# Performance work log

Hardware: AMD Instinct MI355X
Metric: run time of the kernel (lower is better)

Reference implementation:

```python
import jax, jax.numpy as jnp
import numpy as np

T, H, I, E = 8192, 1024, 2816, 8


def setup_inputs() -> dict:
    key = jax.random.key(0)
    k1, k2, k3, k4, k5 = jax.random.split(key, 5)
    s_in = 1.0 / np.sqrt(H)
    s_mid = 1.0 / np.sqrt(I)
    return {
        "x": jax.random.normal(k1, (T, H), dtype=jnp.float32),
        "expert_indices": jax.random.randint(k2, (T,), 0, E),
        "Wg": jax.random.normal(k3, (E, I, H), dtype=jnp.float32) * s_in,
        "Wu": jax.random.normal(k4, (E, I, H), dtype=jnp.float32) * s_in,
        "Wd": jax.random.normal(k5, (E, H, I), dtype=jnp.float32) * s_mid,
    }


def reference(x, expert_indices, Wg, Wu, Wd):
    # Faithful to TPMoEExperts.forward: per-expert 0/1 mask, dense SwiGLU MLP
    # over the full (masked) token batch, masked accumulate into output.
    output = jnp.zeros_like(x)
    for e in range(E):  # small fixed loop over experts (structurally distinct weights)
        mask = (expert_indices == e).astype(x.dtype)[:, None]  # [T,1]
        xi = x * mask                                           # [T,H]
        gate = jax.nn.silu(xi @ Wg[e].T)                        # [T,I]
        up = xi @ Wu[e].T                                       # [T,I]
        out_e = (gate * up) @ Wd[e].T                           # [T,H]
        output = output + out_e * mask
    return output
```

## Files before the change

### kernel.cpp

```cpp
#include <hip/hip_runtime.h>
#include <hip/hip_bf16.h>

#define T_TOK 8192
#define H_DIM 1024
#define I_DIM 2816
#define E_EXP 8

#define BK 64
#define MAXT (T_TOK / 256 + E_EXP)
#define GU_COLS (I_DIM / 128)
#define DN_COLS (H_DIM / 128)

typedef __bf16 bf16x8 __attribute__((ext_vector_type(8)));
typedef float f32x4 __attribute__((ext_vector_type(4)));

#define SWZ(r, bc) (((r) * (BK * 2)) + (((bc) ^ (((r) & 7) << 4))))

__device__ __forceinline__ void gload16(const void* g, void* l) {
  __builtin_amdgcn_global_load_lds((const __attribute__((address_space(1))) void*)g,
                                   (__attribute__((address_space(3))) void*)l, 16, 0, 0);
}

__device__ __forceinline__ bf16x8 cvt8(const float4& p0, const float4& p1) {
  bf16x8 v;
  v[0] = (__bf16)p0.x; v[1] = (__bf16)p0.y; v[2] = (__bf16)p0.z; v[3] = (__bf16)p0.w;
  v[4] = (__bf16)p1.x; v[5] = (__bf16)p1.y; v[6] = (__bf16)p1.z; v[7] = (__bf16)p1.w;
  return v;
}

__device__ __forceinline__ int xcd_swizzle(int id, int nwg) {
  const int q = nwg >> 3, r = nwg & 7;
  const int xcd = id & 7, j = id >> 3;
  return (xcd < r ? xcd * (q + 1) : r * (q + 1) + (xcd - r) * q) + j;
}

__global__ void k_count(const int* __restrict__ idx, int* __restrict__ counts) {
  int t = blockIdx.x * blockDim.x + threadIdx.x;
  if (t < T_TOK) atomicAdd(&counts[idx[t]], 1);
}

__global__ void k_tilesB(const int* __restrict__ counts, int* __restrict__ offsets,
                         int* __restrict__ tE, int* __restrict__ tB,
                         int* __restrict__ tEnd, int* __restrict__ nT) {
  if (threadIdx.x != 0 || blockIdx.x != 0) return;
  int off = 0, nt = 0;
  for (int e = 0; e < E_EXP; ++e) {
    offsets[e] = off;
    int c = counts[e];
    for (int b = 0; b < c; b += 256) { tE[nt] = e; tB[nt] = off + b; tEnd[nt] = off + c; ++nt; }
    off += c;
  }
  offsets[E_EXP] = off;
  *nT = nt;
}

__global__ void k_scatter(const int* __restrict__ idx, const int* __restrict__ offsets,
                          int* __restrict__ cursor, int* __restrict__ order) {
  int t = blockIdx.x * blockDim.x + threadIdx.x;
  if (t < T_TOK) {
    int e = idx[t];
    int p = offsets[e] + atomicAdd(&cursor[e], 1);
    order[p] = t;
  }
}

__global__ __launch_bounds__(256) void k_cvt3(const float* __restrict__ s0, const float* __restrict__ s1,
                                              const float* __restrict__ s2, __bf16* __restrict__ d0,
                                              __bf16* __restrict__ d1, __bf16* __restrict__ d2, int n8each) {
  int i = blockIdx.x * blockDim.x + threadIdx.x;
  int seg = i / n8each;
  int j = i - seg * n8each;
  if (seg >= 3) return;
  const float* s = seg == 0 ? s0 : (seg == 1 ? s1 : s2);
  __bf16* d = seg == 0 ? d0 : (seg == 1 ? d1 : d2);
  const float4 p0 = ((const float4*)s)[j * 2];
  const float4 p1 = ((const float4*)s)[j * 2 + 1];
  ((bf16x8*)d)[j] = cvt8(p0, p1);
}

__global__ __launch_bounds__(128) void k_xperm(const float* __restrict__ x,
                                               const int* __restrict__ order,
                                               __bf16* __restrict__ xp) {
  const int row = blockIdx.x;
  const int tok = order[row];
  const float* s = x + (size_t)tok * H_DIM + threadIdx.x * 8;
  const float4 p0 = ((const float4*)s)[0];
  const float4 p1 = ((const float4*)s)[1];
  *(bf16x8*)(xp + (size_t)row * H_DIM + threadIdx.x * 8) = cvt8(p0, p1);
}

__global__ __launch_bounds__(512, 2) void k_gateup7(
    const __bf16* __restrict__ xp, const __bf16* __restrict__ wg, const __bf16* __restrict__ wu,
    const int* __restrict__ tE, const int* __restrict__ tB,
    const int* __restrict__ tEnd, const int* __restrict__ nT, __bf16* __restrict__ hp) {
  const int nwg = *nT * GU_COLS;
  const int id = blockIdx.x;
  if (id >= nwg) return;
  const int wgid = xcd_swizzle(id, nwg);
  const int tile = wgid / GU_COLS;
  const int col = wgid - tile * GU_COLS;
  const int e = tE[tile];
  const int rowbase = tB[tile];
  const int rowEnd = tEnd[tile];
  const int nbase = col * 128;

  extern __shared__ __align__(16) unsigned char smem[];
  unsigned char* smA = smem;
  unsigned char* smG = smem + 65536;
  unsigned char* smU = smem + 98304;

  const int tid = threadIdx.x;
  const int lane = tid & 63;
  const int w = tid >> 6;
  const int wm = w & 3, wn = w >> 2;

  const int lr = lane >> 3;
  const int lc = (lane & 7) ^ lr;
  const __bf16* aS[4]; const __bf16* gS[2]; const __bf16* uS[2];
  int adst[4], gdst[2];
#pragma unroll
  for (int r = 0; r < 4; ++r) {
    const int rt = r * 64 + w * 8 + lr;
    aS[r] = xp + (size_t)(rowbase + rt) * H_DIM + lc * 8;
    adst[r] = rt * 128;
  }
#pragma unroll
  for (int r = 0; r < 2; ++r) {
    const int rt = r * 64 + w * 8 + lr;
    gS[r] = wg + ((size_t)e * I_DIM + nbase + rt) * H_DIM + lc * 8;
    uS[r] = wu + ((size_t)e * I_DIM + nbase + rt) * H_DIM + lc * 8;
    gdst[r] = rt * 128;
  }

  f32x4 accg[4][4], accu[4][4];
#pragma unroll
  for (int m = 0; m < 4; ++m)
#pragma unroll
    for (int n = 0; n < 4; ++n)
#pragma unroll
      for (int j = 0; j < 4; ++j) { accg[m][n][j] = 0.f; accu[m][n][j] = 0.f; }

  const int nK = H_DIM / BK;
#pragma unroll
  for (int r = 0; r < 4; ++r) gload16(aS[r], smA + adst[r]);
#pragma unroll
  for (int r = 0; r < 2; ++r) {
    gload16(gS[r], smG + gdst[r]);
    gload16(uS[r], smU + gdst[r]);
  }
  __syncthreads();

  int cur = 0;
  for (int kt = 0; kt < nK; ++kt) {
    if (kt + 1 < nK) {
      const int kof = (kt + 1) * BK;
      const int bA = (cur ^ 1) * 32768, bG = (cur ^ 1) * 16384;
#pragma unroll
      for (int r = 0; r < 4; ++r) gload16(aS[r] + kof, smA + bA + adst[r]);
#pragma unroll
      for (int r = 0; r < 2; ++r) {
        gload16(gS[r] + kof, smG + bG + gdst[r]);
        gload16(uS[r] + kof, smU + bG + gdst[r]);
      }
    }
    const unsigned char* A = smA + cur * 32768;
    const unsigned char* G = smG + cur * 16384;
    const unsigned char* U = smU + cur * 16384;
#pragma unroll
    for (int ks = 0; ks < 2; ++ks) {
      const int kc = ks * 64 + ((lane >> 4) * 16);
      bf16x8 a[4], bg[4], bu[4];
#pragma unroll
      for (int m = 0; m < 4; ++m)
        a[m] = *(const bf16x8*)(A + SWZ(wm * 64 + m * 16 + (lane & 15), kc));
#pragma unroll
      for (int n = 0; n < 4; ++n) {
        const int off = SWZ(wn * 64 + n * 16 + (lane & 15), kc);
        bg[n] = *(const bf16x8*)(G + off);
        bu[n] = *(const bf16x8*)(U + off);
      }
#pragma unroll
      for (int m = 0; m < 4; ++m)
#pragma unroll
        for (int n = 0; n < 4; ++n) {
          accg[m][n] = __builtin_amdgcn_mfma_f32_16x16x32_bf16(a[m], bg[n], accg[m][n], 0, 0, 0);
          accu[m][n] = __builtin_amdgcn_mfma_f32_16x16x32_bf16(a[m], bu[n], accu[m][n], 0, 0, 0);
        }
    }
    __syncthreads();
    cur ^= 1;
  }

#pragma unroll
  for (int m = 0; m < 4; ++m) {
    const int row0 = wm * 64 + m * 16 + (lane >> 4) * 4;
#pragma unroll
    for (int j = 0; j < 4; ++j) {
      const int gr = rowbase + row0 + j;
      if (gr < rowEnd) {
        __bf16* dst = hp + (size_t)gr * I_DIM + nbase;
#pragma unroll
        for (int n = 0; n < 4; ++n) {
          const int c2 = wn * 64 + n * 16 + (lane & 15);
          const float g = accg[m][n][j];
          const float u = accu[m][n][j];
          dst[c2] = (__bf16)(g / (1.f + __expf(-g)) * u);
        }
      }
    }
  }
}

__global__ __launch_bounds__(512, 2) void k_down7(
    const __bf16* __restrict__ hp, const __bf16* __restrict__ wd,
    const int* __restrict__ order, const int* __restrict__ tE, const int* __restrict__ tB,
    const int* __restrict__ tEnd, const int* __restrict__ nT, float* __restrict__ out) {
  const int nwg = *nT * DN_COLS;
  const int id = blockIdx.x;
  if (id >= nwg) return;
  const int wgid = xcd_swizzle(id, nwg);
  const int tile = wgid >> 3;
  const int col = wgid & 7;
  const int e = tE[tile];
  const int rowbase = tB[tile];
  const int rowEnd = tEnd[tile];
  const int nbase = col * 128;

  extern __shared__ __align__(16) unsigned char smem2[];
  unsigned char* smA = smem2;
  unsigned char* smB = smem2 + 65536;

  const int tid = threadIdx.x;
  const int lane = tid & 63;
  const int w = tid >> 6;
  const int wm = w & 3, wn = w >> 2;

  const int lr = lane >> 3;
  const int lc = (lane & 7) ^ lr;
  const __bf16* aS[4]; const __bf16* bS[2];
  int adst[4], bdst[2];
#pragma unroll
  for (int r = 0; r < 4; ++r) {
    const int rt = r * 64 + w * 8 + lr;
    aS[r] = hp + (size_t)(rowbase + rt) * I_DIM + lc * 8;
    adst[r] = rt * 128;
  }
#pragma unroll
  for (int r = 0; r < 2; ++r) {
    const int rt = r * 64 + w * 8 + lr;
    bS[r] = wd + ((size_t)e * H_DIM + nbase + rt) * I_DIM + lc * 8;
    bdst[r] = rt * 128;
  }

  f32x4 acc[4][4];
#pragma unroll
  for (int m = 0; m < 4; ++m)
#pragma unroll
    for (int n = 0; n < 4; ++n)
#pragma unroll
      for (int j = 0; j < 4; ++j) acc[m][n][j] = 0.f;

  const int nK = I_DIM / BK;
#pragma unroll
  for (int r = 0; r < 4; ++r) gload16(aS[r], smA + adst[r]);
#pragma unroll
  for (int r = 0; r < 2; ++r) gload16(bS[r], smB + bdst[r]);
  __syncthreads();

  int cur = 0;
  for (int kt = 0; kt < nK; ++kt) {
    if (kt + 1 < nK) {
      const int kof = (kt + 1) * BK;
      const int bA = (cur ^ 1) * 32768, bB = (cur ^ 1) * 16384;
#pragma unroll
      for (int r = 0; r < 4; ++r) gload16(aS[r] + kof, smA + bA + adst[r]);
#pragma unroll
      for (int r = 0; r < 2; ++r) gload16(bS[r] + kof, smB + bB + bdst[r]);
    }
    const unsigned char* A = smA + cur * 32768;
    const unsigned char* B = smB + cur * 16384;
#pragma unroll
    for (int ks = 0; ks < 2; ++ks) {
      const int kc = ks * 64 + ((lane >> 4) * 16);
      bf16x8 a[4], b[4];
#pragma unroll
      for (int m = 0; m < 4; ++m)
        a[m] = *(const bf16x8*)(A + SWZ(wm * 64 + m * 16 + (lane & 15), kc));
#pragma unroll
      for (int n = 0; n < 4; ++n)
        b[n] = *(const bf16x8*)(B + SWZ(wn * 64 + n * 16 + (lane & 15), kc));
#pragma unroll
      for (int m = 0; m < 4; ++m)
#pragma unroll
        for (int n = 0; n < 4; ++n)
          acc[m][n] = __builtin_amdgcn_mfma_f32_16x16x32_bf16(a[m], b[n], acc[m][n], 0, 0, 0);
    }
    __syncthreads();
    cur ^= 1;
  }

#pragma unroll
  for (int m = 0; m < 4; ++m) {
    const int row0 = wm * 64 + m * 16 + (lane >> 4) * 4;
#pragma unroll
    for (int j = 0; j < 4; ++j) {
      const int gr = rowbase + row0 + j;
      if (gr < rowEnd) {
        const int tok = order[gr];
        float* dst = out + (size_t)tok * H_DIM + nbase;
#pragma unroll
        for (int n = 0; n < 4; ++n) {
          const int c2 = wn * 64 + n * 16 + (lane & 15);
          dst[c2] = acc[m][n][j];
        }
      }
    }
  }
}

extern "C" void kernel_launch(void* const* d_in, const int* in_sizes, int n_in,
                              void* d_out, int out_size, void* d_ws, size_t ws_size,
                              hipStream_t stream) {
  const float* x = (const float*)d_in[0];
  const int* eidx = (const int*)d_in[1];
  const float* Wg = (const float*)d_in[2];
  const float* Wu = (const float*)d_in[3];
  const float* Wd = (const float*)d_in[4];
  float* out = (float*)d_out;

  char* ws = (char*)d_ws;
  size_t off = 0;
  auto alloc = [&](size_t bytes) -> void* {
    void* p = ws + off;
    off = (off + bytes + 255) & ~(size_t)255;
    return p;
  };
  const size_t TPAD = T_TOK + 256;
  __bf16* hp = (__bf16*)alloc(TPAD * I_DIM * sizeof(__bf16));
  int* order = (int*)alloc(T_TOK * sizeof(int));
  int* offsets = (int*)alloc((E_EXP + 1) * sizeof(int));
  int* tE = (int*)alloc(MAXT * sizeof(int));
  int* tB = (int*)alloc(MAXT * sizeof(int));
  int* tEnd = (int*)alloc(MAXT * sizeof(int));
  int* nT = (int*)alloc(sizeof(int));
  int* cc = (int*)alloc(2 * E_EXP * sizeof(int));
  int* counts = cc;
  int* cursor = cc + E_EXP;

  const size_t WSZ = (size_t)E_EXP * I_DIM * H_DIM;
  __bf16* xp = (__bf16*)alloc(TPAD * H_DIM * sizeof(__bf16));
  __bf16* wg16 = (__bf16*)alloc(WSZ * sizeof(__bf16));
  __bf16* wu16 = (__bf16*)alloc(WSZ * sizeof(__bf16));
  __bf16* wd16 = (__bf16*)alloc(WSZ * sizeof(__bf16));

  hipFuncSetAttribute((const void*)k_gateup7,
                      hipFuncAttributeMaxDynamicSharedMemorySize, 131072);
  hipFuncSetAttribute((const void*)k_down7,
                      hipFuncAttributeMaxDynamicSharedMemorySize, 98304);

  hipMemsetAsync(cc, 0, 2 * E_EXP * sizeof(int), stream);
  k_count<<<T_TOK / 256, 256, 0, stream>>>(eidx, counts);
  k_tilesB<<<1, 1, 0, stream>>>(counts, offsets, tE, tB, tEnd, nT);
  k_scatter<<<T_TOK / 256, 256, 0, stream>>>(eidx, offsets, cursor, order);

  const int n8 = (int)(WSZ / 8);
  k_cvt3<<<(3 * n8 + 255) / 256, 256, 0, stream>>>(Wg, Wu, Wd, wg16, wu16, wd16, n8);
  k_xperm<<<T_TOK, 128, 0, stream>>>(x, order, xp);

  k_gateup7<<<GU_COLS * MAXT, 512, 131072, stream>>>(xp, wg16, wu16, tE, tB, tEnd, nT, hp);
  k_down7<<<DN_COLS * MAXT, 512, 98304, stream>>>(hp, wd16, order, tE, tB, tEnd, nT, out);
}
```

Baseline: 373.0 us.

## Restructure down-projection pipeline into half-K stages with fine-grained waitcnt barriers

Rewrites the down-projection GEMM main loop to split each 64-wide K tile into two 32-wide halves. Each half is staged with direct-to-LDS loads, and the loop waits with explicit vmcnt counts and raw s_barrier instead of a full __syncthreads. The warp layout changes to 4x2, the LDS swizzle is new, and MFMA sections are wrapped in s_setprio. The aim is to overlap global loads with MFMA work more tightly and to cut synchronisation stalls. It also drops the occupancy hint in launch_bounds and relies on hand-counted vmcnt values, which risks races if the counts are wrong.

```diff
diff --git a/kernel.cpp b/kernel.cpp
--- a/kernel.cpp
+++ b/kernel.cpp
@@ -32,6 +32,13 @@
   const int q = nwg >> 3, r = nwg & 7;
   const int xcd = id & 7, j = id >> 3;
   return (xcd < r ? xcd * (q + 1) : r * (q + 1) + (xcd - r) * q) + j;
+}
+
+#define FENCE() asm volatile("" ::: "memory")
+#define BARRIER() do { __builtin_amdgcn_s_barrier(); FENCE(); } while (0)
+
+__device__ __forceinline__ int swz_off(int row, int lane) {
+  return row * 64 + ((((lane >> 4)) ^ ((row >> 1) & 3)) << 4);
 }
 
 __global__ void k_count(const int* __restrict__ idx, int* __restrict__ counts) {
@@ -211,7 +218,7 @@
   }
 }
 
-__global__ __launch_bounds__(512, 2) void k_down7(
+__global__ __launch_bounds__(512) void k_down10(
     const __bf16* __restrict__ hp, const __bf16* __restrict__ wd,
     const int* __restrict__ order, const int* __restrict__ tE, const int* __restrict__ tB,
     const int* __restrict__ tEnd, const int* __restrict__ nT, float* __restrict__ out) {
@@ -228,29 +235,19 @@
 
   extern __shared__ __align__(16) unsigned char smem2[];
   unsigned char* smA = smem2;
-  unsigned char* smB = smem2 + 65536;
+  unsigned char* smW = smem2 + 65536;
 
   const int tid = threadIdx.x;
   const int lane = tid & 63;
   const int w = tid >> 6;
-  const int wm = w & 3, wn = w >> 2;
-
-  const int lr = lane >> 3;
-  const int lc = (lane & 7) ^ lr;
-  const __bf16* aS[4]; const __bf16* bS[2];
-  int adst[4], bdst[2];
-#pragma unroll
-  for (int r = 0; r < 4; ++r) {
-    const int rt = r * 64 + w * 8 + lr;
-    aS[r] = hp + (size_t)(rowbase + rt) * I_DIM + lc * 8;
-    adst[r] = rt * 128;
-  }
-#pragma unroll
-  for (int r = 0; r < 2; ++r) {
-    const int rt = r * 64 + w * 8 + lr;
-    bS[r] = wd + ((size_t)e * H_DIM + nbase + rt) * I_DIM + lc * 8;
-    bdst[r] = rt * 128;
-  }
+  const int wm = w >> 1, wn = w & 1;
+
+  const int srow = tid >> 2;
+  const int sch = (tid & 3) ^ ((tid >> 3) & 3);
+  const __bf16* aS0 = hp + (size_t)(rowbase + srow) * I_DIM + sch * 8;
+  const __bf16* aS1 = aS0 + (size_t)128 * I_DIM;
+  const __bf16* wS = wd + ((size_t)e * H_DIM + nbase + srow) * I_DIM + sch * 8;
+  const int ldst = tid * 16;
 
   f32x4 acc[4][4];
 #pragma unroll
@@ -260,48 +257,57 @@
 #pragma unroll
       for (int j = 0; j < 4; ++j) acc[m][n][j] = 0.f;
 
-  const int nK = I_DIM / BK;
-#pragma unroll
-  for (int r = 0; r < 4; ++r) gload16(aS[r], smA + adst[r]);
-#pragma unroll
-  for (int r = 0; r < 2; ++r) gload16(bS[r], smB + bdst[r]);
-  __syncthreads();
-
-  int cur = 0;
-  for (int kt = 0; kt < nK; ++kt) {
-    if (kt + 1 < nK) {
-      const int kof = (kt + 1) * BK;
-      const int bA = (cur ^ 1) * 32768, bB = (cur ^ 1) * 16384;
-#pragma unroll
-      for (int r = 0; r < 4; ++r) gload16(aS[r] + kof, smA + bA + adst[r]);
-#pragma unroll
-      for (int r = 0; r < 2; ++r) gload16(bS[r] + kof, smB + bB + bdst[r]);
-    }
-    const unsigned char* A = smA + cur * 32768;
-    const unsigned char* B = smB + cur * 16384;
-#pragma unroll
-    for (int ks = 0; ks < 2; ++ks) {
-      const int kc = ks * 64 + ((lane >> 4) * 16);
-      bf16x8 a[4], b[4];
-#pragma unroll
-      for (int m = 0; m < 4; ++m)
-        a[m] = *(const bf16x8*)(A + SWZ(wm * 64 + m * 16 + (lane & 15), kc));
+  auto STAGE = [&](int t1, int kh) {
+    const int b = t1 & 1;
+    const size_t ko = (size_t)t1 * 64 + kh * 32;
+    gload16(aS0 + ko, smA + (b * 2 + kh) * 16384 + ldst);
+    gload16(aS1 + ko, smA + (b * 2 + kh) * 16384 + 8192 + ldst);
+    gload16(wS + ko, smW + (b * 2 + kh) * 8192 + ldst);
+  };
+
+  auto COMPUTE = [&](int buf, int kh) {
+    const unsigned char* A = smA + (buf * 2 + kh) * 16384;
+    const unsigned char* W = smW + (buf * 2 + kh) * 8192;
+    bf16x8 a[4], b[4];
+#pragma unroll
+    for (int m = 0; m < 4; ++m)
+      a[m] = *(const bf16x8*)(A + swz_off(wm * 64 + m * 16 + (lane & 15), lane));
+#pragma unroll
+    for (int n = 0; n < 4; ++n)
+      b[n] = *(const bf16x8*)(W + swz_off(wn * 64 + n * 16 + (lane & 15), lane));
+    __builtin_amdgcn_s_setprio(1);
+#pragma unroll
+    for (int m = 0; m < 4; ++m)
 #pragma unroll
       for (int n = 0; n < 4; ++n)
-        b[n] = *(const bf16x8*)(B + SWZ(wn * 64 + n * 16 + (lane & 15), kc));
-#pragma unroll
-      for (int m = 0; m < 4; ++m)
-#pragma unroll
-        for (int n = 0; n < 4; ++n)
-          acc[m][n] = __builtin_amdgcn_mfma_f32_16x16x32_bf16(a[m], b[n], acc[m][n], 0, 0, 0);
-    }
-    __syncthreads();
-    cur ^= 1;
+        acc[m][n] = __builtin_amdgcn_mfma_f32_16x16x32_bf16(a[m], b[n], acc[m][n], 0, 0, 0);
+    __builtin_amdgcn_s_setprio(0);
+  };
+
+  const int nK = I_DIM / 64;
+  STAGE(0, 0);
+  STAGE(0, 1);
+  asm volatile("s_waitcnt vmcnt(3)" ::: "memory");
+  BARRIER();
+
+  for (int t = 0; t < nK; ++t) {
+    const int buf = t & 1;
+    const bool pf = (t + 1 < nK);
+    if (pf) STAGE(t + 1, 0);
+    COMPUTE(buf, 0);
+    if (pf) asm volatile("s_waitcnt vmcnt(3)" ::: "memory");
+    else    asm volatile("s_waitcnt vmcnt(0)" ::: "memory");
+    BARRIER();
+    if (pf) STAGE(t + 1, 1);
+    COMPUTE(buf, 1);
+    if (pf) asm volatile("s_waitcnt vmcnt(3)" ::: "memory");
+    else    asm volatile("s_waitcnt vmcnt(0)" ::: "memory");
+    BARRIER();
   }
 
 #pragma unroll
   for (int m = 0; m < 4; ++m) {
-    const int row0 = wm * 64 + m * 16 + (lane >> 4) * 4;
+    const int row0 = wm * 64 + m * 16 + ((lane >> 4) << 2);
 #pragma unroll
     for (int j = 0; j < 4; ++j) {
       const int gr = rowbase + row0 + j;
@@ -355,7 +361,7 @@
 
   hipFuncSetAttribute((const void*)k_gateup7,
                       hipFuncAttributeMaxDynamicSharedMemorySize, 131072);
-  hipFuncSetAttribute((const void*)k_down7,
+  hipFuncSetAttribute((const void*)k_down10,
                       hipFuncAttributeMaxDynamicSharedMemorySize, 98304);
 
   hipMemsetAsync(cc, 0, 2 * E_EXP * sizeof(int), stream);
@@ -368,5 +374,5 @@
   k_xperm<<<T_TOK, 128, 0, stream>>>(x, order, xp);
 
   k_gateup7<<<GU_COLS * MAXT, 512, 131072, stream>>>(xp, wg16, wu16, tE, tB, tEnd, nT, hp);
-  k_down7<<<DN_COLS * MAXT, 512, 98304, stream>>>(hp, wd16, order, tE, tB, tEnd, nT, out);
-}
+  k_down10<<<MAXT * DN_COLS, 512, 98304, stream>>>(hp, wd16, order, tE, tB, tEnd, nT, out);
+}
```

Result: no change. 366.4 us (-1.8%).
